# Performance work log

Hardware: AMD Instinct MI355X
Metric: run time of the kernel (lower is better)

The kernel has to match this reference:

```python
import jax, jax.numpy as jnp
import numpy as np

B, S, H, F = 256, 196, 1024, 2048  # batch, att_size, hidden/att_hid, att_feat_size


def setup_inputs() -> dict:
    key = jax.random.key(0)
    ks = jax.random.split(key, 10)
    sc = 1.0 / np.sqrt(H)
    return {
        "ha": jax.random.normal(ks[0], (B, H), jnp.float32),
        "hf": jax.random.normal(ks[1], (B, H), jnp.float32),
        "att_feats": jax.random.normal(ks[2], (B, S, F), jnp.float32),
        "p_att_feats": jax.random.normal(ks[3], (B, S, H), jnp.float32),
        "W_ha": jax.random.normal(ks[4], (H, H), jnp.float32) * sc,
        "b_ha": jax.random.normal(ks[5], (H,), jnp.float32) * sc,
        "W_hf": jax.random.normal(ks[6], (H, H), jnp.float32) * sc,
        "b_hf": jax.random.normal(ks[7], (H,), jnp.float32) * sc,
        "w_alpha": jax.random.normal(ks[8], (H,), jnp.float32) * sc,
        "b_alpha": jax.random.normal(ks[9], (1,), jnp.float32) * sc,
    }


def reference(ha, hf, att_feats, p_att_feats, W_ha, b_ha, W_hf, b_hf, w_alpha, b_alpha):
    # additive (Bahdanau-style) attention with two query projections
    att_ha = ha @ W_ha.T + b_ha          # [B, H]
    att_hf = hf @ W_hf.T + b_hf          # [B, H]
    dot = jnp.tanh(att_ha[:, None, :] + att_hf[:, None, :] + p_att_feats)  # [B, S, H]
    scores = jnp.einsum("bsh,h->bs", dot, w_alpha) + b_alpha[0]            # [B, S]
    weight = jax.nn.softmax(scores, axis=1)                                 # [B, S]
    att_res = jnp.einsum("bs,bsf->bf", weight, att_feats)                   # [B, F]
    return att_res
```

## Files before the change

### kernel.cpp

```cpp
#include <hip/hip_runtime.h>
#include <hip/hip_bf16.h>
#include <hip/hip_fp16.h>

#define Bdim 256
#define Sdim 196
#define Hdim 1024
#define Fdim 2048
#define BH (Bdim*Hdim)
#define L2E 1.44269504f
#define C2L 2.88539008f

typedef float nfloat4 __attribute__((ext_vector_type(4)));

__device__ __forceinline__ float4 ldnt4(const float* p) {
    nfloat4 v = __builtin_nontemporal_load(reinterpret_cast<const nfloat4*>(p));
    return make_float4(v.x, v.y, v.z, v.w);
}

#define TM 128
#define TN 128
#define TK 32

__global__ __launch_bounds__(256) void gemm_q_part(
    const float* __restrict__ ha, const float* __restrict__ hf,
    const float* __restrict__ Wha, const float* __restrict__ Whf,
    __half* __restrict__ qpart, int kchunk)
{
    __shared__ float As[TK][TM + 4];
    __shared__ float Ws[TK][TN + 4];

    const int tid = threadIdx.x;
    const int th  = tid & 15;
    const int tb  = tid >> 4;
    const int h0  = blockIdx.x * TN;
    const int b0  = blockIdx.y * TM;
    const int z   = blockIdx.z;
    const int kv_base = z * kchunk;

    float acc[8][8];
    #pragma unroll
    for (int i = 0; i < 8; ++i)
        #pragma unroll
        for (int j = 0; j < 8; ++j) acc[i][j] = 0.0f;

    float4 xv[4], wv[4];

    auto load_regs = [&](int t) {
        int kv = kv_base + t * TK;
        const float* X; const float* W; int k0;
        if (kv < 1024) { X = ha; W = Wha; k0 = kv; }
        else           { X = hf; W = Whf; k0 = kv - 1024; }
        #pragma unroll
        for (int r = 0; r < 4; ++r) {
            int idx = tid + r * 256;
            int row = idx >> 3, kq = idx & 7;
            xv[r] = *reinterpret_cast<const float4*>(X + (size_t)(b0 + row) * Hdim + k0 + kq * 4);
            wv[r] = *reinterpret_cast<const float4*>(W + (size_t)(h0 + row) * Hdim + k0 + kq * 4);
        }
    };

    const int ntiles = kchunk / TK;
    load_regs(0);

    for (int t = 0; t < ntiles; ++t) {
        #pragma unroll
        for (int r = 0; r < 4; ++r) {
            int idx = tid + r * 256;
            int row = idx >> 3, kq = idx & 7;
            As[kq * 4 + 0][row] = xv[r].x;
            As[kq * 4 + 1][row] = xv[r].y;
            As[kq * 4 + 2][row] = xv[r].z;
            As[kq * 4 + 3][row] = xv[r].w;
            Ws[kq * 4 + 0][row] = wv[r].x;
            Ws[kq * 4 + 1][row] = wv[r].y;
            Ws[kq * 4 + 2][row] = wv[r].z;
            Ws[kq * 4 + 3][row] = wv[r].w;
        }
        __syncthreads();

        if (t + 1 < ntiles) load_regs(t + 1);

        #pragma unroll
        for (int k = 0; k < TK; ++k) {
            float4 a0 = *reinterpret_cast<const float4*>(&As[k][tb * 8]);
            float4 a1 = *reinterpret_cast<const float4*>(&As[k][tb * 8 + 4]);
            float4 w0 = *reinterpret_cast<const float4*>(&Ws[k][th * 8]);
            float4 w1 = *reinterpret_cast<const float4*>(&Ws[k][th * 8 + 4]);
            float a[8] = {a0.x, a0.y, a0.z, a0.w, a1.x, a1.y, a1.z, a1.w};
            float w[8] = {w0.x, w0.y, w0.z, w0.w, w1.x, w1.y, w1.z, w1.w};
            #pragma unroll
            for (int i = 0; i < 8; ++i)
                #pragma unroll
                for (int j = 0; j < 8; ++j)
                    acc[i][j] += a[i] * w[j];
        }
        __syncthreads();
    }

    #pragma unroll
    for (int i = 0; i < 8; ++i) {
        int b = b0 + tb * 8 + i;
        __half* dst = qpart + (size_t)z * BH + (size_t)b * Hdim + h0 + th * 8;
        __half2* dst2 = reinterpret_cast<__half2*>(dst);
        dst2[0] = __floats2half2_rn(acc[i][0], acc[i][1]);
        dst2[1] = __floats2half2_rn(acc[i][2], acc[i][3]);
        dst2[2] = __floats2half2_rn(acc[i][4], acc[i][5]);
        dst2[3] = __floats2half2_rn(acc[i][6], acc[i][7]);
    }
}

__global__ __launch_bounds__(1024) void fused_kernel(
    const __half* __restrict__ qpart, const float* __restrict__ b_ha,
    const float* __restrict__ b_hf,  const float* __restrict__ p_att,
    const float* __restrict__ w_alpha, const float* __restrict__ b_alpha,
    const float* __restrict__ att_feats, float* __restrict__ out, int ks)
{
    __shared__ __align__(16) float qt[4 * Hdim];
    __shared__ __align__(16) float wa_s[Hdim];
    __shared__ __align__(16) float sc[Sdim];
    __shared__ __align__(16) float part[Fdim];
    __shared__ float wred[4];

    const int b    = blockIdx.x;
    const int tid  = threadIdx.x;
    const int wave = tid >> 6, lane = tid & 63;

    {
        const int zg = tid >> 8;
        const int h4 = tid & 255;
        size_t off = (size_t)b * Hdim + h4 * 4;
        float4 s = {0.f, 0.f, 0.f, 0.f};
        for (int z = zg; z < ks; z += 4) {
            const __half2* p2 = reinterpret_cast<const __half2*>(qpart + (size_t)z * BH + off);
            float2 f0 = __half22float2(p2[0]);
            float2 f1 = __half22float2(p2[1]);
            s.x += f0.x; s.y += f0.y; s.z += f1.x; s.w += f1.y;
        }
        if (zg == 0) {
            float4 ba = *reinterpret_cast<const float4*>(b_ha + h4 * 4);
            float4 bb = *reinterpret_cast<const float4*>(b_hf + h4 * 4);
            s.x += ba.x + bb.x; s.y += ba.y + bb.y;
            s.z += ba.z + bb.z; s.w += ba.w + bb.w;
        }
        *reinterpret_cast<float4*>(qt + zg * Hdim + h4 * 4) = s;
        if (zg == 1) {
            float4 w = *reinterpret_cast<const float4*>(w_alpha + h4 * 4);
            *reinterpret_cast<float4*>(wa_s + h4 * 4) = w;
            float ls = w.x + w.y + w.z + w.w;
            #pragma unroll
            for (int m = 32; m >= 1; m >>= 1) ls += __shfl_xor(ls, m, 64);
            if (lane == 0) wred[wave - 4] = ls;
        }
    }
    __syncthreads();

    const float base_sc = wred[0] + wred[1] + wred[2] + wred[3] + b_alpha[0];

    float4 qr[4], wr[4];
    #pragma unroll
    for (int i = 0; i < 4; ++i) {
        const int idx = (i * 64 + lane) * 4;
        float4 s0 = *reinterpret_cast<const float4*>(qt + idx);
        float4 s1 = *reinterpret_cast<const float4*>(qt + Hdim + idx);
        float4 s2 = *reinterpret_cast<const float4*>(qt + 2 * Hdim + idx);
        float4 s3 = *reinterpret_cast<const float4*>(qt + 3 * Hdim + idx);
        qr[i].x = (s0.x + s1.x + s2.x + s3.x) * C2L;
        qr[i].y = (s0.y + s1.y + s2.y + s3.y) * C2L;
        qr[i].z = (s0.z + s1.z + s2.z + s3.z) * C2L;
        qr[i].w = (s0.w + s1.w + s2.w + s3.w) * C2L;
        wr[i] = *reinterpret_cast<const float4*>(wa_s + idx);
    }

    const float* pbase = p_att + (size_t)b * Sdim * Hdim;
    {
        int s = wave;
        float4 pv[4];
        #pragma unroll
        for (int i = 0; i < 4; ++i)
            pv[i] = ldnt4(pbase + (size_t)s * Hdim + (i * 64 + lane) * 4);
        while (s < Sdim) {
            const int sn = s + 16;
            float4 pn[4];
            if (sn < Sdim) {
                #pragma unroll
                for (int i = 0; i < 4; ++i)
                    pn[i] = ldnt4(pbase + (size_t)sn * Hdim + (i * 64 + lane) * 4);
            }
            float psum = 0.0f;
            #pragma unroll
            for (int i = 0; i < 4; ++i) {
                psum += wr[i].x * __builtin_amdgcn_rcpf(__builtin_amdgcn_exp2f(fmaf(pv[i].x, C2L, qr[i].x)) + 1.0f);
                psum += wr[i].y * __builtin_amdgcn_rcpf(__builtin_amdgcn_exp2f(fmaf(pv[i].y, C2L, qr[i].y)) + 1.0f);
                psum += wr[i].z * __builtin_amdgcn_rcpf(__builtin_amdgcn_exp2f(fmaf(pv[i].z, C2L, qr[i].z)) + 1.0f);
                psum += wr[i].w * __builtin_amdgcn_rcpf(__builtin_amdgcn_exp2f(fmaf(pv[i].w, C2L, qr[i].w)) + 1.0f);
            }
            #pragma unroll
            for (int m = 32; m >= 1; m >>= 1) psum += __shfl_xor(psum, m, 64);
            if (lane == 0) sc[s] = base_sc - 2.0f * psum;
            #pragma unroll
            for (int i = 0; i < 4; ++i) pv[i] = pn[i];
            s = sn;
        }
    }
    __syncthreads();

    float m_max, ssum;
    {
        float v0 = sc[lane];
        float v1 = sc[lane + 64];
        float v2 = sc[lane + 128];
        float v3 = (lane < Sdim - 192) ? sc[lane + 192] : -1e30f;
        float m = fmaxf(fmaxf(v0, v1), fmaxf(v2, v3));
        #pragma unroll
        for (int mk = 32; mk >= 1; mk >>= 1) m = fmaxf(m, __shfl_xor(m, mk, 64));
        float e0 = __builtin_amdgcn_exp2f((v0 - m) * L2E);
        float e1 = __builtin_amdgcn_exp2f((v1 - m) * L2E);
        float e2 = __builtin_amdgcn_exp2f((v2 - m) * L2E);
        float e3 = (lane < Sdim - 192) ? __builtin_amdgcn_exp2f((v3 - m) * L2E) : 0.0f;
        float ss = e0 + e1 + e2 + e3;
        #pragma unroll
        for (int mk = 32; mk >= 1; mk >>= 1) ss += __shfl_xor(ss, mk, 64);
        m_max = m; ssum = ss;
    }

    const int half = tid >> 9;
    const int fi   = (tid & 511) * 4;
    const float* abase = att_feats + (size_t)b * Sdim * Fdim + fi;
    float4 a4 = {0.f, 0.f, 0.f, 0.f};
    const int s0 = half ? 96 : 0;
    const int s1 = half ? 196 : 96;
    int s4 = s0;
    for (; s4 + 8 <= s1; s4 += 8) {
        float4 sa = *reinterpret_cast<const float4*>(sc + s4);
        float4 sb = *reinterpret_cast<const float4*>(sc + s4 + 4);
        float4 v0 = ldnt4(abase + (size_t)(s4 + 0) * Fdim);
        float4 v1 = ldnt4(abase + (size_t)(s4 + 1) * Fdim);
        float4 v2 = ldnt4(abase + (size_t)(s4 + 2) * Fdim);
        float4 v3 = ldnt4(abase + (size_t)(s4 + 3) * Fdim);
        float4 v4 = ldnt4(abase + (size_t)(s4 + 4) * Fdim);
        float4 v5 = ldnt4(abase + (size_t)(s4 + 5) * Fdim);
        float4 v6 = ldnt4(abase + (size_t)(s4 + 6) * Fdim);
        float4 v7 = ldnt4(abase + (size_t)(s4 + 7) * Fdim);
        float e0 = __builtin_amdgcn_exp2f((sa.x - m_max) * L2E);
        float e1 = __builtin_amdgcn_exp2f((sa.y - m_max) * L2E);
        float e2 = __builtin_amdgcn_exp2f((sa.z - m_max) * L2E);
        float e3 = __builtin_amdgcn_exp2f((sa.w - m_max) * L2E);
        float e4 = __builtin_amdgcn_exp2f((sb.x - m_max) * L2E);
        float e5 = __builtin_amdgcn_exp2f((sb.y - m_max) * L2E);
        float e6 = __builtin_amdgcn_exp2f((sb.z - m_max) * L2E);
        float e7 = __builtin_amdgcn_exp2f((sb.w - m_max) * L2E);
        a4.x += e0 * v0.x; a4.y += e0 * v0.y; a4.z += e0 * v0.z; a4.w += e0 * v0.w;
        a4.x += e1 * v1.x; a4.y += e1 * v1.y; a4.z += e1 * v1.z; a4.w += e1 * v1.w;
        a4.x += e2 * v2.x; a4.y += e2 * v2.y; a4.z += e2 * v2.z; a4.w += e2 * v2.w;
        a4.x += e3 * v3.x; a4.y += e3 * v3.y; a4.z += e3 * v3.z; a4.w += e3 * v3.w;
        a4.x += e4 * v4.x; a4.y += e4 * v4.y; a4.z += e4 * v4.z; a4.w += e4 * v4.w;
        a4.x += e5 * v5.x; a4.y += e5 * v5.y; a4.z += e5 * v5.z; a4.w += e5 * v5.w;
        a4.x += e6 * v6.x; a4.y += e6 * v6.y; a4.z += e6 * v6.z; a4.w += e6 * v6.w;
        a4.x += e7 * v7.x; a4.y += e7 * v7.y; a4.z += e7 * v7.z; a4.w += e7 * v7.w;
    }
    if (s4 < s1) {
        float4 sa = *reinterpret_cast<const float4*>(sc + s4);
        float4 v0 = ldnt4(abase + (size_t)(s4 + 0) * Fdim);
        float4 v1 = ldnt4(abase + (size_t)(s4 + 1) * Fdim);
        float4 v2 = ldnt4(abase + (size_t)(s4 + 2) * Fdim);
        float4 v3 = ldnt4(abase + (size_t)(s4 + 3) * Fdim);
        float e0 = __builtin_amdgcn_exp2f((sa.x - m_max) * L2E);
        float e1 = __builtin_amdgcn_exp2f((sa.y - m_max) * L2E);
        float e2 = __builtin_amdgcn_exp2f((sa.z - m_max) * L2E);
        float e3 = __builtin_amdgcn_exp2f((sa.w - m_max) * L2E);
        a4.x += e0 * v0.x; a4.y += e0 * v0.y; a4.z += e0 * v0.z; a4.w += e0 * v0.w;
        a4.x += e1 * v1.x; a4.y += e1 * v1.y; a4.z += e1 * v1.z; a4.w += e1 * v1.w;
        a4.x += e2 * v2.x; a4.y += e2 * v2.y; a4.z += e2 * v2.z; a4.w += e2 * v2.w;
        a4.x += e3 * v3.x; a4.y += e3 * v3.y; a4.z += e3 * v3.z; a4.w += e3 * v3.w;
    }
    if (half) {
        *reinterpret_cast<float4*>(part + fi) = a4;
    }
    __syncthreads();
    if (!half) {
        const float winv = __builtin_amdgcn_rcpf(ssum);
        float4 p4 = *reinterpret_cast<const float4*>(part + fi);
        a4.x = (a4.x + p4.x) * winv; a4.y = (a4.y + p4.y) * winv;
        a4.z = (a4.z + p4.z) * winv; a4.w = (a4.w + p4.w) * winv;
        *reinterpret_cast<float4*>(out + (size_t)b * Fdim + fi) = a4;
    }
}

extern "C" void kernel_launch(void* const* d_in, const int* in_sizes, int n_in,
                              void* d_out, int out_size, void* d_ws, size_t ws_size,
                              hipStream_t stream) {
    const float* ha       = (const float*)d_in[0];
    const float* hf       = (const float*)d_in[1];
    const float* att_f    = (const float*)d_in[2];
    const float* p_att    = (const float*)d_in[3];
    const float* W_ha     = (const float*)d_in[4];
    const float* b_ha     = (const float*)d_in[5];
    const float* W_hf     = (const float*)d_in[6];
    const float* b_hf     = (const float*)d_in[7];
    const float* w_alpha  = (const float*)d_in[8];
    const float* b_alpha  = (const float*)d_in[9];
    float* out = (float*)d_out;
    __half* qpart = (__half*)d_ws;

    int KS = 32;
    while (KS > 1 && ((size_t)KS * BH) * sizeof(__half) > ws_size) KS >>= 1;

    dim3 gA(Hdim / TN, Bdim / TM, KS);
    gemm_q_part<<<gA, 256, 0, stream>>>(ha, hf, W_ha, W_hf, qpart, 2048 / KS);

    fused_kernel<<<dim3(Bdim), 1024, 0, stream>>>(
        qpart, b_ha, b_hf, p_att, w_alpha, b_alpha, att_f, out, KS);
}
```

Baseline: 120.5 us.

## Replace FP32 FMA query-projection GEMM with fp16 MFMA kernel and split-K of 16

The query projection GEMM now converts ha/hf and the weights to fp16 while staging them into XOR-swizzled LDS tiles, and computes with 16x16x32 f16 MFMA instructions in place of scalar FP32 FMAs. Split-K drops from 32 to a fixed 16 with a 128-wide K chunk per block. Results go through an LDS bounce buffer so each thread can write coalesced 16-byte fp16 rows. The aim is to cut GEMM compute time and the partial-sum traffic the fused kernel has to reduce. In exchange, inputs are quantised to fp16, which lowers precision, and the workspace-size check that used to limit KS is gone.

```diff
diff --git a/kernel.cpp b/kernel.cpp
--- a/kernel.cpp
+++ b/kernel.cpp
@@ -9,103 +9,135 @@
 #define BH (Bdim*Hdim)
 #define L2E 1.44269504f
 #define C2L 2.88539008f
+#define KSPLIT 16
 
 typedef float nfloat4 __attribute__((ext_vector_type(4)));
+typedef _Float16 half8 __attribute__((ext_vector_type(8)));
+typedef float f32x4 __attribute__((ext_vector_type(4)));
 
 __device__ __forceinline__ float4 ldnt4(const float* p) {
     nfloat4 v = __builtin_nontemporal_load(reinterpret_cast<const nfloat4*>(p));
     return make_float4(v.x, v.y, v.z, v.w);
 }
 
-#define TM 128
-#define TN 128
-#define TK 32
-
-__global__ __launch_bounds__(256) void gemm_q_part(
+__global__ __launch_bounds__(256) void gemm_q_mfma(
     const float* __restrict__ ha, const float* __restrict__ hf,
     const float* __restrict__ Wha, const float* __restrict__ Whf,
-    __half* __restrict__ qpart, int kchunk)
+    __half* __restrict__ qpart)
 {
-    __shared__ float As[TK][TM + 4];
-    __shared__ float Ws[TK][TN + 4];
-
-    const int tid = threadIdx.x;
-    const int th  = tid & 15;
-    const int tb  = tid >> 4;
-    const int h0  = blockIdx.x * TN;
-    const int b0  = blockIdx.y * TM;
-    const int z   = blockIdx.z;
-    const int kv_base = z * kchunk;
-
-    float acc[8][8];
+    __shared__ __align__(16) _Float16 As[128 * 64];
+    __shared__ __align__(16) _Float16 Bs[128 * 64];
+    __shared__ __align__(16) float bounce[128 * 132];
+
+    const int tid  = threadIdx.x;
+    const int lane = tid & 63;
+    const int wave = tid >> 6;
+    const int wr   = wave >> 1;
+    const int wc   = wave & 1;
+    const int h0   = blockIdx.x * 128;
+    const int b0   = blockIdx.y * 128;
+    const int z    = blockIdx.z;
+    const int kv   = z * 128;
+
+    const float* X; const float* W; int k0;
+    if (kv < 1024) { X = ha; W = Wha; k0 = kv; }
+    else           { X = hf; W = Whf; k0 = kv - 1024; }
+
+    f32x4 acc[4][4];
     #pragma unroll
-    for (int i = 0; i < 8; ++i)
-        #pragma unroll
-        for (int j = 0; j < 8; ++j) acc[i][j] = 0.0f;
-
-    float4 xv[4], wv[4];
-
-    auto load_regs = [&](int t) {
-        int kv = kv_base + t * TK;
-        const float* X; const float* W; int k0;
-        if (kv < 1024) { X = ha; W = Wha; k0 = kv; }
-        else           { X = hf; W = Whf; k0 = kv - 1024; }
-        #pragma unroll
-        for (int r = 0; r < 4; ++r) {
-            int idx = tid + r * 256;
-            int row = idx >> 3, kq = idx & 7;
-            xv[r] = *reinterpret_cast<const float4*>(X + (size_t)(b0 + row) * Hdim + k0 + kq * 4);
-            wv[r] = *reinterpret_cast<const float4*>(W + (size_t)(h0 + row) * Hdim + k0 + kq * 4);
+    for (int m = 0; m < 4; ++m)
+        #pragma unroll
+        for (int n = 0; n < 4; ++n) acc[m][n] = (f32x4){0.f, 0.f, 0.f, 0.f};
+
+    float4 xa[8], xb[8];
+
+    auto issue_loads = [&](int khalf) {
+        const int kh = k0 + khalf * 64;
+        #pragma unroll
+        for (int i = 0; i < 8; ++i) {
+            int u = tid + i * 256;
+            int row = u >> 4, c4 = u & 15;
+            xa[i] = *reinterpret_cast<const float4*>(X + (size_t)(b0 + row) * Hdim + kh + c4 * 4);
+            xb[i] = *reinterpret_cast<const float4*>(W + (size_t)(h0 + row) * Hdim + kh + c4 * 4);
         }
     };
 
-    const int ntiles = kchunk / TK;
-    load_regs(0);
-
-    for (int t = 0; t < ntiles; ++t) {
-        #pragma unroll
-        for (int r = 0; r < 4; ++r) {
-            int idx = tid + r * 256;
-            int row = idx >> 3, kq = idx & 7;
-            As[kq * 4 + 0][row] = xv[r].x;
-            As[kq * 4 + 1][row] = xv[r].y;
-            As[kq * 4 + 2][row] = xv[r].z;
-            As[kq * 4 + 3][row] = xv[r].w;
-            Ws[kq * 4 + 0][row] = wv[r].x;
-            Ws[kq * 4 + 1][row] = wv[r].y;
-            Ws[kq * 4 + 2][row] = wv[r].z;
-            Ws[kq * 4 + 3][row] = wv[r].w;
-        }
-        __syncthreads();
-
-        if (t + 1 < ntiles) load_regs(t + 1);
-
-        #pragma unroll
-        for (int k = 0; k < TK; ++k) {
-            float4 a0 = *reinterpret_cast<const float4*>(&As[k][tb * 8]);
-            float4 a1 = *reinterpret_cast<const float4*>(&As[k][tb * 8 + 4]);
-            float4 w0 = *reinterpret_cast<const float4*>(&Ws[k][th * 8]);
-            float4 w1 = *reinterpret_cast<const float4*>(&Ws[k][th * 8 + 4]);
-            float a[8] = {a0.x, a0.y, a0.z, a0.w, a1.x, a1.y, a1.z, a1.w};
-            float w[8] = {w0.x, w0.y, w0.z, w0.w, w1.x, w1.y, w1.z, w1.w};
-            #pragma unroll
-            for (int i = 0; i < 8; ++i)
+    auto st4h = [&](_Float16* base, int byte, float4 v) {
+        _Float16 t[4] = {(_Float16)v.x, (_Float16)v.y, (_Float16)v.z, (_Float16)v.w};
+        *reinterpret_cast<uint2*>(reinterpret_cast<char*>(base) + byte) =
+            *reinterpret_cast<uint2*>(t);
+    };
+
+    auto write_lds = [&]() {
+        #pragma unroll
+        for (int i = 0; i < 8; ++i) {
+            int u = tid + i * 256;
+            int row = u >> 4, c4 = u & 15;
+            int byte = row * 128 + ((c4 * 8) ^ ((row & 7) << 4));
+            st4h(As, byte, xa[i]);
+            st4h(Bs, byte, xb[i]);
+        }
+    };
+
+    auto mfma_half = [&]() {
+        #pragma unroll
+        for (int kk = 0; kk < 2; ++kk) {
+            half8 af[4], bf[4];
+            const int k8 = kk * 4 + (lane >> 4);
+            #pragma unroll
+            for (int m = 0; m < 4; ++m) {
+                int row = wr * 64 + m * 16 + (lane & 15);
+                int byte = row * 128 + ((k8 * 16) ^ ((row & 7) << 4));
+                af[m] = *reinterpret_cast<half8*>(reinterpret_cast<char*>(As) + byte);
+            }
+            #pragma unroll
+            for (int n = 0; n < 4; ++n) {
+                int row = wc * 64 + n * 16 + (lane & 15);
+                int byte = row * 128 + ((k8 * 16) ^ ((row & 7) << 4));
+                bf[n] = *reinterpret_cast<half8*>(reinterpret_cast<char*>(Bs) + byte);
+            }
+            #pragma unroll
+            for (int m = 0; m < 4; ++m)
                 #pragma unroll
-                for (int j = 0; j < 8; ++j)
-                    acc[i][j] += a[i] * w[j];
-        }
-        __syncthreads();
-    }
-
+                for (int n = 0; n < 4; ++n)
+                    acc[m][n] = __builtin_amdgcn_mfma_f32_16x16x32_f16(
+                        af[m], bf[n], acc[m][n], 0, 0, 0);
+        }
+    };
+
+    issue_loads(0);
+    write_lds();
+    __syncthreads();
+    issue_loads(1);
+    mfma_half();
+    __syncthreads();
+    write_lds();
+    __syncthreads();
+    mfma_half();
+
+    #pragma unroll
+    for (int m = 0; m < 4; ++m)
+        #pragma unroll
+        for (int n = 0; n < 4; ++n)
+            #pragma unroll
+            for (int j = 0; j < 4; ++j) {
+                int r = wr * 64 + m * 16 + (lane >> 4) * 4 + j;
+                int c = wc * 64 + n * 16 + (lane & 15);
+                bounce[r * 132 + c] = acc[m][n][j];
+            }
+    __syncthreads();
+
+    __half* qbase = qpart + (size_t)z * BH;
     #pragma unroll
     for (int i = 0; i < 8; ++i) {
-        int b = b0 + tb * 8 + i;
-        __half* dst = qpart + (size_t)z * BH + (size_t)b * Hdim + h0 + th * 8;
-        __half2* dst2 = reinterpret_cast<__half2*>(dst);
-        dst2[0] = __floats2half2_rn(acc[i][0], acc[i][1]);
-        dst2[1] = __floats2half2_rn(acc[i][2], acc[i][3]);
-        dst2[2] = __floats2half2_rn(acc[i][4], acc[i][5]);
-        dst2[3] = __floats2half2_rn(acc[i][6], acc[i][7]);
+        int u = tid + i * 256;
+        int row = u >> 4, ch = u & 15;
+        const float* src = bounce + row * 132 + ch * 8;
+        __half2 p[4];
+        #pragma unroll
+        for (int j = 0; j < 4; ++j) p[j] = __floats2half2_rn(src[2 * j], src[2 * j + 1]);
+        *reinterpret_cast<float4*>(qbase + (size_t)(b0 + row) * Hdim + h0 + ch * 8) =
+            *reinterpret_cast<float4*>(p);
     }
 }
 
@@ -302,12 +334,9 @@
     float* out = (float*)d_out;
     __half* qpart = (__half*)d_ws;
 
-    int KS = 32;
-    while (KS > 1 && ((size_t)KS * BH) * sizeof(__half) > ws_size) KS >>= 1;
-
-    dim3 gA(Hdim / TN, Bdim / TM, KS);
-    gemm_q_part<<<gA, 256, 0, stream>>>(ha, hf, W_ha, W_hf, qpart, 2048 / KS);
+    dim3 gA(Hdim / 128, Bdim / 128, KSPLIT);
+    gemm_q_mfma<<<gA, 256, 0, stream>>>(ha, hf, W_ha, W_hf, qpart);
 
     fused_kernel<<<dim3(Bdim), 1024, 0, stream>>>(
-        qpart, b_ha, b_hf, p_att, w_alpha, b_alpha, att_f, out, KS);
+        qpart, b_ha, b_hf, p_att, w_alpha, b_alpha, att_f, out, KSPLIT);
 }
```

Result: faster. 108.7 us (-9.8%).
